# Kernel tuning notes

Hardware: AMD Instinct MI355X
Metric: run time of the kernel (lower is better)

Reference implementation:

```python
import jax, jax.numpy as jnp
import numpy as np

EMB_SIZE = 100000
EMB_DIM = 256
HALF = EMB_DIM // 2
B = 65536
K = 5


def setup_inputs() -> dict:
    key = jax.random.key(0)
    ks = jax.random.split(key, 9)
    initrange = 1.0 / EMB_DIM
    u_l = jax.random.uniform(ks[0], (EMB_SIZE, HALF), jnp.float32, -initrange, initrange)
    u_r = jax.random.uniform(ks[1], (EMB_SIZE, HALF), jnp.float32, -initrange, initrange)
    # torch init is zeros for v tables; use small random so grads/outputs are nontrivial
    v_l = jax.random.uniform(ks[2], (EMB_SIZE, HALF), jnp.float32, -initrange, initrange)
    v_r = jax.random.uniform(ks[3], (EMB_SIZE, HALF), jnp.float32, -initrange, initrange)
    pos_u = jax.random.randint(ks[4], (B,), 0, EMB_SIZE)
    pos_v_l = jax.random.randint(ks[5], (B,), 0, EMB_SIZE)
    pos_v_r = jax.random.randint(ks[6], (B,), 0, EMB_SIZE)
    neg_v_l = jax.random.randint(ks[7], (B, K), 0, EMB_SIZE)
    neg_v_r = jax.random.randint(ks[8], (B, K), 0, EMB_SIZE)
    return {
        "u_l_weight": u_l, "u_r_weight": u_r,
        "v_l_weight": v_l, "v_r_weight": v_r,
        "pos_u": pos_u, "pos_v_l": pos_v_l, "pos_v_r": pos_v_r,
        "neg_v_l": neg_v_l, "neg_v_r": neg_v_r,
    }


def _neg_logsig(x):
    # -logsigmoid(x), numerically stable
    return -jax.nn.log_sigmoid(x)


def reference(u_l_weight, u_r_weight, v_l_weight, v_r_weight,
              pos_u, pos_v_l, pos_v_r, neg_v_l, neg_v_r):
    emb_u_l = u_l_weight[pos_u]          # [B, H]
    emb_u_r = u_r_weight[pos_u]          # [B, H]
    emb_v_l = v_l_weight[pos_v_l]        # [B, H]
    emb_v_r = v_r_weight[pos_v_r]        # [B, H]
    emb_neg_v_l = v_l_weight[neg_v_l]    # [B, K, H]
    emb_neg_v_r = v_r_weight[neg_v_r]    # [B, K, H]

    score_l = jnp.clip(jnp.sum(emb_u_l * emb_v_l, axis=1), -10.0, 10.0)
    score_l = _neg_logsig(score_l)
    score_r = jnp.clip(jnp.sum(emb_u_r * emb_v_r, axis=1), -10.0, 10.0)
    score_r = _neg_logsig(score_r)

    neg_score_l = jnp.clip(jnp.einsum('bkh,bh->bk', emb_neg_v_l, emb_u_l), -10.0, 10.0)
    neg_score_l = -jnp.sum(jax.nn.log_sigmoid(-neg_score_l), axis=1)
    neg_score_r = jnp.clip(jnp.einsum('bkh,bh->bk', emb_neg_v_r, emb_u_r), -10.0, 10.0)
    neg_score_r = -jnp.sum(jax.nn.log_sigmoid(-neg_score_r), axis=1)

    return jnp.mean(score_l + score_r + neg_score_l + neg_score_r)
```

## Files before the change

kernel.cpp:

```cpp
#include <hip/hip_runtime.h>
#include <stdint.h>


#define HV     128
#define BATCH  65536
#define K      5
#define NBLK   1024
#define WPB    4
#define ITERS  (BATCH / (NBLK * WPB))
#define WBUF   (14 * HV)

struct Idx { int iu, ivl, ivr, nl[K], nr[K]; };

__device__ __forceinline__ Idx load_idx(const int* pu, const int* pvl, const int* pvr,
                                        const int* nvl, const int* nvr, int b) {
    Idx x;
    x.iu  = pu[b];  x.ivl = pvl[b];  x.ivr = pvr[b];
    #pragma unroll
    for (int k = 0; k < K; ++k) { x.nl[k] = nvl[b*K + k]; x.nr[k] = nvr[b*K + k]; }
    return x;
}

__device__ __forceinline__ void dma_pair(const float* rowA, const float* rowB,
                                         float* ldsBase, int lane) {
    const float* g = ((lane < 32) ? rowA : rowB) + (lane & 31) * 4;
    __builtin_amdgcn_global_load_lds(
        (const __attribute__((address_space(1))) void*)g,
        (__attribute__((address_space(3))) void*)ldsBase,
        16, 0, 0);
}

__device__ __forceinline__ float2 rd2(const float* buf, int off, int lane) {
    return *(const float2*)(buf + off + 2 * lane);
}
__device__ __forceinline__ float dot2(float2 a, float2 b) { return a.x*b.x + a.y*b.y; }
__device__ __forceinline__ float clip10(float x) { return fminf(fmaxf(x, -10.f), 10.f); }

__global__ __launch_bounds__(256) void skipgram_fwd(
    const float* __restrict__ u_l, const float* __restrict__ u_r,
    const float* __restrict__ v_l, const float* __restrict__ v_r,
    const int* __restrict__ pos_u, const int* __restrict__ pos_vl,
    const int* __restrict__ pos_vr, const int* __restrict__ neg_vl,
    const int* __restrict__ neg_vr, float* __restrict__ out)
{
    __shared__ float stage[WPB][WBUF];
    __shared__ float wsum[WPB];

    const int tid  = threadIdx.x;
    const int lane = tid & 63;
    const int wv   = tid >> 6;
    const int b0   = (blockIdx.x * WPB + wv) * ITERS;
    float* buf = &stage[wv][0];

    float acc = 0.0f;
    Idx cur = load_idx(pos_u, pos_vl, pos_vr, neg_vl, neg_vr, b0);

    for (int it = 0; it < ITERS; ++it) {
        dma_pair(u_l + (size_t)cur.iu   * HV, u_r + (size_t)cur.iu   * HV, buf + 0*256, lane);
        dma_pair(v_l + (size_t)cur.ivl  * HV, v_r + (size_t)cur.ivr  * HV, buf + 1*256, lane);
        dma_pair(v_l + (size_t)cur.nl[0]* HV, v_l + (size_t)cur.nl[1]* HV, buf + 2*256, lane);
        dma_pair(v_l + (size_t)cur.nl[2]* HV, v_l + (size_t)cur.nl[3]* HV, buf + 3*256, lane);
        dma_pair(v_l + (size_t)cur.nl[4]* HV, v_r + (size_t)cur.nr[0]* HV, buf + 4*256, lane);
        dma_pair(v_r + (size_t)cur.nr[1]* HV, v_r + (size_t)cur.nr[2]* HV, buf + 5*256, lane);
        dma_pair(v_r + (size_t)cur.nr[3]* HV, v_r + (size_t)cur.nr[4]* HV, buf + 6*256, lane);

        const int bn = b0 + ((it + 1 < ITERS) ? (it + 1) : 0);
        Idx nxt = load_idx(pos_u, pos_vl, pos_vr, neg_vl, neg_vr, bn);

        __builtin_amdgcn_s_waitcnt(0x0F70);
        __builtin_amdgcn_sched_barrier(0);

        float2 u2l = rd2(buf, 0,   lane);
        float2 u2r = rd2(buf, 128, lane);
        float s[12];
        s[0] = dot2(u2l, rd2(buf, 256, lane));
        s[1] = dot2(u2r, rd2(buf, 384, lane));
        #pragma unroll
        for (int k = 0; k < K; ++k) {
            s[2 + k] = dot2(u2l, rd2(buf,  512 + 128*k, lane));
            s[7 + k] = dot2(u2r, rd2(buf, 1152 + 128*k, lane));
        }
        #pragma unroll
        for (int m = 1; m < 64; m <<= 1) {
            #pragma unroll
            for (int j = 0; j < 12; ++j) s[j] += __shfl_xor(s[j], m, 64);
        }
        acc += __logf(1.0f + __expf(-clip10(s[0])));
        acc += __logf(1.0f + __expf(-clip10(s[1])));
        #pragma unroll
        for (int j = 2; j < 12; ++j)
            acc += __logf(1.0f + __expf(clip10(s[j])));

        cur = nxt;
    }

    if (lane == 0) wsum[wv] = acc;
    __syncthreads();
    if (tid == 0) {
        float s = wsum[0] + wsum[1] + wsum[2] + wsum[3];
        atomicAdd(out, s * (1.0f / BATCH));
    }
}

extern "C" void kernel_launch(void* const* d_in, const int* in_sizes, int n_in,
                              void* d_out, int out_size, void* d_ws, size_t ws_size,
                              hipStream_t stream) {
    const float* u_l   = (const float*)d_in[0];
    const float* u_r   = (const float*)d_in[1];
    const float* v_l   = (const float*)d_in[2];
    const float* v_r   = (const float*)d_in[3];
    const int* pos_u   = (const int*)d_in[4];
    const int* pos_vl  = (const int*)d_in[5];
    const int* pos_vr  = (const int*)d_in[6];
    const int* neg_vl  = (const int*)d_in[7];
    const int* neg_vr  = (const int*)d_in[8];
    float* out = (float*)d_out;

    hipMemsetAsync(out, 0, sizeof(float), stream);

    skipgram_fwd<<<NBLK, 256, 0, stream>>>(
        u_l, u_r, v_l, v_r, pos_u, pos_vl, pos_vr, neg_vl, neg_vr, out);
}
```

Measured before the change: 237.1 us.

## Double-buffer LDS row gathers and preload per-wave indices into shared memory

Each wave now preloads all 16 batch items' indices into LDS up front, then keeps two LDS staging buffers so the gather DMA for the next item is in flight while the current item is reduced. Previously every iteration waited for its own gather to finish, and only the index loads for the next item were overlapped. Blocks shrink to 2 waves with 16 items per wave (2048 blocks), and LDS use per wave roughly doubles. This may reduce how many waves fit on a CU.

```diff
diff --git a/kernel.cpp b/kernel.cpp
--- a/kernel.cpp
+++ b/kernel.cpp
@@ -5,21 +5,11 @@
 #define HV     128
 #define BATCH  65536
 #define K      5
-#define NBLK   1024
-#define WPB    4
-#define ITERS  (BATCH / (NBLK * WPB))
+#define WPB    2
+#define ITERS  16
+#define NBLK   (BATCH / (WPB * ITERS))
 #define WBUF   (14 * HV)
-
-struct Idx { int iu, ivl, ivr, nl[K], nr[K]; };
-
-__device__ __forceinline__ Idx load_idx(const int* pu, const int* pvl, const int* pvr,
-                                        const int* nvl, const int* nvr, int b) {
-    Idx x;
-    x.iu  = pu[b];  x.ivl = pvl[b];  x.ivr = pvr[b];
-    #pragma unroll
-    for (int k = 0; k < K; ++k) { x.nl[k] = nvl[b*K + k]; x.nr[k] = nvr[b*K + k]; }
-    return x;
-}
+#define NIDX   (3 * 16 + 2 * 16 * K)
 
 __device__ __forceinline__ void dma_pair(const float* rowA, const float* rowB,
                                          float* ldsBase, int lane) {
@@ -36,68 +26,104 @@
 __device__ __forceinline__ float dot2(float2 a, float2 b) { return a.x*b.x + a.y*b.y; }
 __device__ __forceinline__ float clip10(float x) { return fminf(fmaxf(x, -10.f), 10.f); }
 
-__global__ __launch_bounds__(256) void skipgram_fwd(
+__device__ __forceinline__ void issue_group(
+    const float* u_l, const float* u_r, const float* v_l, const float* v_r,
+    const int* ix, int it, float* buf, int lane)
+{
+    const int iu  = ix[it];
+    const int ivl = ix[16 + it];
+    const int ivr = ix[32 + it];
+    const int o   = 48  + it * K;
+    const int p   = 128 + it * K;
+    dma_pair(u_l + (size_t)iu       * HV, u_r + (size_t)iu       * HV, buf + 0*256, lane);
+    dma_pair(v_l + (size_t)ivl      * HV, v_r + (size_t)ivr      * HV, buf + 1*256, lane);
+    dma_pair(v_l + (size_t)ix[o+0]  * HV, v_l + (size_t)ix[o+1]  * HV, buf + 2*256, lane);
+    dma_pair(v_l + (size_t)ix[o+2]  * HV, v_l + (size_t)ix[o+3]  * HV, buf + 3*256, lane);
+    dma_pair(v_l + (size_t)ix[o+4]  * HV, v_r + (size_t)ix[p+0]  * HV, buf + 4*256, lane);
+    dma_pair(v_r + (size_t)ix[p+1]  * HV, v_r + (size_t)ix[p+2]  * HV, buf + 5*256, lane);
+    dma_pair(v_r + (size_t)ix[p+3]  * HV, v_r + (size_t)ix[p+4]  * HV, buf + 6*256, lane);
+}
+
+__device__ __forceinline__ float consume(const float* buf, int lane) {
+    float2 ul = rd2(buf, 0,   lane);
+    float2 ur = rd2(buf, 128, lane);
+    float s[12];
+    s[0] = dot2(ul, rd2(buf, 256, lane));
+    s[1] = dot2(ur, rd2(buf, 384, lane));
+    #pragma unroll
+    for (int k = 0; k < K; ++k) {
+        s[2 + k] = dot2(ul, rd2(buf,  512 + 128*k, lane));
+        s[7 + k] = dot2(ur, rd2(buf, 1152 + 128*k, lane));
+    }
+    #pragma unroll
+    for (int m = 1; m < 64; m <<= 1) {
+        #pragma unroll
+        for (int j = 0; j < 12; ++j) s[j] += __shfl_xor(s[j], m, 64);
+    }
+    float a = __logf(1.f + __expf(-clip10(s[0])))
+            + __logf(1.f + __expf(-clip10(s[1])));
+    #pragma unroll
+    for (int j = 2; j < 12; ++j)
+        a += __logf(1.f + __expf(clip10(s[j])));
+    return a;
+}
+
+__global__ __launch_bounds__(128) void skipgram_fwd(
     const float* __restrict__ u_l, const float* __restrict__ u_r,
     const float* __restrict__ v_l, const float* __restrict__ v_r,
     const int* __restrict__ pos_u, const int* __restrict__ pos_vl,
     const int* __restrict__ pos_vr, const int* __restrict__ neg_vl,
     const int* __restrict__ neg_vr, float* __restrict__ out)
 {
-    __shared__ float stage[WPB][WBUF];
+    __shared__ float bufA[WPB][WBUF];
+    __shared__ float bufB[WPB][WBUF];
+    __shared__ int   idx[WPB][NIDX];
     __shared__ float wsum[WPB];
 
     const int tid  = threadIdx.x;
     const int lane = tid & 63;
     const int wv   = tid >> 6;
     const int b0   = (blockIdx.x * WPB + wv) * ITERS;
-    float* buf = &stage[wv][0];
 
+    for (int i = lane; i < NIDX; i += 64) {
+        int v;
+        if      (i < 16)  v = pos_u [b0 + i];
+        else if (i < 32)  v = pos_vl[b0 + i - 16];
+        else if (i < 48)  v = pos_vr[b0 + i - 32];
+        else if (i < 128) v = neg_vl[b0 * K + i - 48];
+        else              v = neg_vr[b0 * K + i - 128];
+        idx[wv][i] = v;
+    }
+    __builtin_amdgcn_s_waitcnt(0x0070);
+
+    const int* ix = idx[wv];
+    float* bA = &bufA[wv][0];
+    float* bB = &bufB[wv][0];
     float acc = 0.0f;
-    Idx cur = load_idx(pos_u, pos_vl, pos_vr, neg_vl, neg_vr, b0);
 
-    for (int it = 0; it < ITERS; ++it) {
-        dma_pair(u_l + (size_t)cur.iu   * HV, u_r + (size_t)cur.iu   * HV, buf + 0*256, lane);
-        dma_pair(v_l + (size_t)cur.ivl  * HV, v_r + (size_t)cur.ivr  * HV, buf + 1*256, lane);
-        dma_pair(v_l + (size_t)cur.nl[0]* HV, v_l + (size_t)cur.nl[1]* HV, buf + 2*256, lane);
-        dma_pair(v_l + (size_t)cur.nl[2]* HV, v_l + (size_t)cur.nl[3]* HV, buf + 3*256, lane);
-        dma_pair(v_l + (size_t)cur.nl[4]* HV, v_r + (size_t)cur.nr[0]* HV, buf + 4*256, lane);
-        dma_pair(v_r + (size_t)cur.nr[1]* HV, v_r + (size_t)cur.nr[2]* HV, buf + 5*256, lane);
-        dma_pair(v_r + (size_t)cur.nr[3]* HV, v_r + (size_t)cur.nr[4]* HV, buf + 6*256, lane);
-
-        const int bn = b0 + ((it + 1 < ITERS) ? (it + 1) : 0);
-        Idx nxt = load_idx(pos_u, pos_vl, pos_vr, neg_vl, neg_vr, bn);
-
-        __builtin_amdgcn_s_waitcnt(0x0F70);
+    issue_group(u_l, u_r, v_l, v_r, ix, 0, bA, lane);
+    for (int it = 0; it + 2 < ITERS; it += 2) {
+        issue_group(u_l, u_r, v_l, v_r, ix, it + 1, bB, lane);
+        __builtin_amdgcn_s_waitcnt(0x0F77);
         __builtin_amdgcn_sched_barrier(0);
-
-        float2 u2l = rd2(buf, 0,   lane);
-        float2 u2r = rd2(buf, 128, lane);
-        float s[12];
-        s[0] = dot2(u2l, rd2(buf, 256, lane));
-        s[1] = dot2(u2r, rd2(buf, 384, lane));
-        #pragma unroll
-        for (int k = 0; k < K; ++k) {
-            s[2 + k] = dot2(u2l, rd2(buf,  512 + 128*k, lane));
-            s[7 + k] = dot2(u2r, rd2(buf, 1152 + 128*k, lane));
-        }
-        #pragma unroll
-        for (int m = 1; m < 64; m <<= 1) {
-            #pragma unroll
-            for (int j = 0; j < 12; ++j) s[j] += __shfl_xor(s[j], m, 64);
-        }
-        acc += __logf(1.0f + __expf(-clip10(s[0])));
-        acc += __logf(1.0f + __expf(-clip10(s[1])));
-        #pragma unroll
-        for (int j = 2; j < 12; ++j)
-            acc += __logf(1.0f + __expf(clip10(s[j])));
-
-        cur = nxt;
+        acc += consume(bA, lane);
+        issue_group(u_l, u_r, v_l, v_r, ix, it + 2, bA, lane);
+        __builtin_amdgcn_s_waitcnt(0x0F77);
+        __builtin_amdgcn_sched_barrier(0);
+        acc += consume(bB, lane);
     }
+    issue_group(u_l, u_r, v_l, v_r, ix, ITERS - 1, bB, lane);
+    __builtin_amdgcn_s_waitcnt(0x0F77);
+    __builtin_amdgcn_sched_barrier(0);
+    acc += consume(bA, lane);
+    __builtin_amdgcn_s_waitcnt(0x0F70);
+    __builtin_amdgcn_sched_barrier(0);
+    acc += consume(bB, lane);
 
     if (lane == 0) wsum[wv] = acc;
     __syncthreads();
     if (tid == 0) {
-        float s = wsum[0] + wsum[1] + wsum[2] + wsum[3];
+        float s = wsum[0] + wsum[1];
         atomicAdd(out, s * (1.0f / BATCH));
     }
 }
@@ -118,6 +144,6 @@
 
     hipMemsetAsync(out, 0, sizeof(float), stream);
 
-    skipgram_fwd<<<NBLK, 256, 0, stream>>>(
+    skipgram_fwd<<<NBLK, 128, 0, stream>>>(
         u_l, u_r, v_l, v_r, pos_u, pos_vl, pos_vr, neg_vl, neg_vr, out);
 }
```

New measurement: 255.1 us. 1.08x slower.
